# Kernel tuning notes

Hardware: AMD Instinct MI355X
Metric: run time of the kernel (lower is better)

## Reference

```python
import jax, jax.numpy as jnp
import numpy as np

N_NODES = 100_000
N_RAND_EDGES = 3_200_000
IN_FEATS, HIDDEN, N_CLASSES = 256, 32, 40


def setup_inputs() -> dict:
    key = jax.random.key(0)
    kf, ks, kd, kw1, kw2 = jax.random.split(key, 5)
    features = jax.random.normal(kf, (N_NODES, IN_FEATS), dtype=jnp.float32)
    # random edges + explicit self loops (mirrors dgl.add_self_loop)
    src = jnp.concatenate([
        jax.random.randint(ks, (N_RAND_EDGES,), 0, N_NODES, dtype=jnp.int32),
        jnp.arange(N_NODES, dtype=jnp.int32),
    ])
    dst = jnp.concatenate([
        jax.random.randint(kd, (N_RAND_EDGES,), 0, N_NODES, dtype=jnp.int32),
        jnp.arange(N_NODES, dtype=jnp.int32),
    ])
    # Glorot-style init as in DGL GraphConv
    W1 = jax.random.normal(kw1, (IN_FEATS, HIDDEN), dtype=jnp.float32) * (2.0 / (IN_FEATS + HIDDEN)) ** 0.5
    b1 = jnp.zeros((HIDDEN,), dtype=jnp.float32)
    W2 = jax.random.normal(kw2, (HIDDEN, N_CLASSES), dtype=jnp.float32) * (2.0 / (HIDDEN + N_CLASSES)) ** 0.5
    b2 = jnp.zeros((N_CLASSES,), dtype=jnp.float32)
    return {"features": features, "src": src, "dst": dst,
            "W1": W1, "b1": b1, "W2": W2, "b2": b2}


def _graph_conv(x, W, b, src, dst, norm_src, norm_dst):
    """DGL GraphConv, norm='both': D_in^{-1/2} A D_out^{-1/2} X W + b.
    Apply W first (cheaper gather when out_feats small); math-identical."""
    h = (x * norm_src[:, None]) @ W              # [N, out]
    msgs = h[src]                                # gather  [E, out]
    agg = jax.ops.segment_sum(msgs, dst, num_segments=N_NODES)  # scatter-add
    return agg * norm_dst[:, None] + b


def reference(features, src, dst, W1, b1, W2, b2):
    ones = jnp.ones(src.shape[0], dtype=jnp.float32)
    out_deg = jax.ops.segment_sum(ones, src, num_segments=N_NODES)
    in_deg = jax.ops.segment_sum(ones, dst, num_segments=N_NODES)
    norm_src = jax.lax.rsqrt(out_deg)            # self loops guarantee deg >= 1
    norm_dst = jax.lax.rsqrt(in_deg)

    x = _graph_conv(features, W1, b1, src, dst, norm_src, norm_dst)
    x = jax.nn.relu(x)
    # F.dropout(training=self.training) is identity at inference
    x = _graph_conv(x, W2, b2, src, dst, norm_src, norm_dst)
    return jax.nn.log_softmax(x, axis=1)
```

## Files before the change

kernel.cpp:

```cpp
#include <hip/hip_runtime.h>
#include <hip/hip_bf16.h>
#include <math.h>

#define BSHIFT 7
#define NBUCK(N) (((N) + 127) >> 7)
#define TILE 8192
#define CAP 5632
#define CAPS 2040
#define NXCD 8

typedef short bf16x8 __attribute__((ext_vector_type(8)));
typedef float f32x16 __attribute__((ext_vector_type(16)));

__device__ __forceinline__ unsigned short f2bf(float f) {
    unsigned u = __float_as_uint(f);
    u += 0x7fffu + ((u >> 16) & 1u);
    return (unsigned short)(u >> 16);
}
__device__ __forceinline__ unsigned packbf2(float lo, float hi) {
    return (unsigned)f2bf(lo) | ((unsigned)f2bf(hi) << 16);
}
__device__ __forceinline__ float bf_lo(unsigned u) { return __uint_as_float(u << 16); }
__device__ __forceinline__ float bf_hi(unsigned u) { return __uint_as_float(u & 0xffff0000u); }

__device__ __forceinline__ int xcc_id() {
    int x;
    asm volatile("s_getreg_b32 %0, hwreg(HW_REG_XCC_ID)" : "=s"(x));
    return x & (NXCD - 1);
}

__global__ __launch_bounds__(256) void pg_kernel(
    const int* __restrict__ src, const int* __restrict__ dst,
    int* __restrict__ gcurD, int* __restrict__ gcurS,
    int* __restrict__ gbufD, unsigned char* __restrict__ gbufS,
    const float* __restrict__ feat, const float* __restrict__ W1,
    unsigned short* __restrict__ h1, int E, int K, int PB, int N) {
    __shared__ char smem[16896];
    const int t = threadIdx.x;

    if (blockIdx.x < PB) {
        int* cD = (int*)smem;
        int* bD = cD + 800;
        int* cS = bD + 800;
        int* bS = cS + 800;
        const int tile = blockIdx.x * TILE;
        const int vx = xcc_id();
        for (int i = t; i < K; i += 256) { cD[i] = 0; cS[i] = 0; }
        __syncthreads();

        int dv[32];
        #pragma unroll
        for (int i = 0; i < 32; ++i) {
            const int e = tile + i * 256 + t;
            dv[i] = (e < E) ? dst[e] : -1;
            if (dv[i] >= 0) {
                atomicAdd(&cD[dv[i] >> BSHIFT], 1);
                atomicAdd(&cS[src[e] >> BSHIFT], 1);
            }
        }
        __syncthreads();
        for (int i = t; i < K; i += 256) {
            int c = cD[i];
            bD[i] = (c ? atomicAdd(&gcurD[i], c) : 0) + i * CAP;
            cD[i] = 0;
            c = cS[i];
            bS[i] = (c ? atomicAdd(&gcurS[vx * K + i], c) : 0) + (vx * K + i) * CAPS;
            cS[i] = 0;
        }
        __syncthreads();
        #pragma unroll
        for (int i = 0; i < 32; ++i) {
            if (dv[i] >= 0) {
                const int e = tile + i * 256 + t;
                const int sv = src[e];
                const int b1 = dv[i] >> BSHIFT;
                const int p1 = bD[b1] + atomicAdd(&cD[b1], 1);
                gbufD[p1] = ((dv[i] & 127) << 17) | sv;
                const int b2 = sv >> BSHIFT;
                const int p2 = bS[b2] + atomicAdd(&cS[b2], 1);
                gbufS[p2] = (unsigned char)(sv & 127);
            }
        }
    } else {
        short* W1t = (short*)smem;
        for (int i = t; i < 8192; i += 256) {
            const int k = i >> 5, c = i & 31;
            W1t[c * 264 + k] = (short)f2bf(W1[i]);
        }
        __syncthreads();

        const int l  = t & 63;
        const int wv = t >> 6;
        const int base = (blockIdx.x - PB) * 128 + wv * 32;
        const int m  = l & 31;
        const int kh = (l >> 5) << 3;
        int r = base + m;
        if (r >= N) r = N - 1;
        const float* fr = feat + (size_t)r * 256 + kh;
        const short* wr = &W1t[m * 264 + kh];

        f32x16 acc;
        #pragma unroll
        for (int i = 0; i < 16; ++i) acc[i] = 0.f;

        #pragma unroll
        for (int kb = 0; kb < 16; ++kb) {
            const float4 f0 = *(const float4*)(fr + kb * 16);
            const float4 f1 = *(const float4*)(fr + kb * 16 + 4);
            bf16x8 a;
            a[0] = (short)f2bf(f0.x); a[1] = (short)f2bf(f0.y);
            a[2] = (short)f2bf(f0.z); a[3] = (short)f2bf(f0.w);
            a[4] = (short)f2bf(f1.x); a[5] = (short)f2bf(f1.y);
            a[6] = (short)f2bf(f1.z); a[7] = (short)f2bf(f1.w);
            const bf16x8 b = *(const bf16x8*)(wr + kb * 16);
            acc = __builtin_amdgcn_mfma_f32_32x32x16_bf16(a, b, acc, 0, 0, 0);
        }

        const int rbase = base + ((l >> 5) << 2);
        #pragma unroll
        for (int reg = 0; reg < 16; ++reg) {
            const int row = rbase + (reg & 3) + ((reg >> 2) << 3);
            if (row < N)
                h1[(size_t)row * 32 + m] = f2bf(acc[reg]);
        }
    }
}

__global__ __launch_bounds__(256) void fillS_kernel(
    const int* __restrict__ cntS, const unsigned char* __restrict__ gbufS,
    float* __restrict__ nsrc, unsigned* __restrict__ h1, int N, int K) {
    __shared__ int cnt[128];
    __shared__ float sns[128];
    const int t = threadIdx.x;
    const int b = blockIdx.x;
    if (t < 128) cnt[t] = 0;
    __syncthreads();
    for (int x = 0; x < NXCD; ++x) {
        const int seg = x * K + b;
        const int bs = seg * CAPS;
        const int be = bs + min(cntS[seg], CAPS);
        for (int idx = bs + t; idx < be; idx += 256)
            atomicAdd(&cnt[gbufS[idx]], 1);
    }
    __syncthreads();
    if (t < 128) {
        const float v = rsqrtf((float)cnt[t]);
        sns[t] = v;
        const int n = (b << BSHIFT) + t;
        if (n < N) nsrc[n] = v;
    }
    __syncthreads();
    const int node = t >> 1;
    const int n = (b << BSHIFT) + node;
    if (n < N) {
        const float ns = sns[node];
        unsigned* row = h1 + (size_t)n * 16 + (t & 1) * 8;
        uint4 q0 = *(uint4*)row;
        uint4 q1 = *(uint4*)(row + 4);
        q0.x = packbf2(bf_lo(q0.x) * ns, bf_hi(q0.x) * ns);
        q0.y = packbf2(bf_lo(q0.y) * ns, bf_hi(q0.y) * ns);
        q0.z = packbf2(bf_lo(q0.z) * ns, bf_hi(q0.z) * ns);
        q0.w = packbf2(bf_lo(q0.w) * ns, bf_hi(q0.w) * ns);
        q1.x = packbf2(bf_lo(q1.x) * ns, bf_hi(q1.x) * ns);
        q1.y = packbf2(bf_lo(q1.y) * ns, bf_hi(q1.y) * ns);
        q1.z = packbf2(bf_lo(q1.z) * ns, bf_hi(q1.z) * ns);
        q1.w = packbf2(bf_lo(q1.w) * ns, bf_hi(q1.w) * ns);
        *(uint4*)row = q0;
        *(uint4*)(row + 4) = q1;
    }
}

__global__ __launch_bounds__(512) void fda1_kernel(
    const int* __restrict__ cntD, int* __restrict__ gbufD,
    const unsigned* __restrict__ h1, const float* __restrict__ nsrc,
    const float* __restrict__ b1, int* __restrict__ rowstart,
    int* __restrict__ indeg, float* __restrict__ ndst,
    unsigned* __restrict__ x1s, int N, int K) {
    __shared__ int lraw[CAP];
    __shared__ int lcsr[CAP];
    __shared__ int cnt[512], sc[512], cur[512];
    __shared__ float sb1[32];
    const int t = threadIdx.x;
    const int b = blockIdx.x;
    if (t < 512) cnt[t] = 0;
    if (t < 32) sb1[t] = b1[t];
    __syncthreads();

    const int bs = b * CAP;
    const int total = min(cntD[b], CAP);
    for (int i = t; i < total; i += 512) {
        const int v = gbufD[bs + i];
        lraw[i] = v;
        const int key = ((v >> 17) << 2) | ((v & 131071) >> 15);
        atomicAdd(&cnt[key], 1);
    }
    __syncthreads();
    sc[t] = cnt[t];
    __syncthreads();
    for (int off = 1; off < 512; off <<= 1) {
        int x = (t >= off) ? sc[t - off] : 0;
        __syncthreads();
        sc[t] += x;
        __syncthreads();
    }
    cur[t] = sc[t] - cnt[t];
    if (t < 128) {
        const int rsl = sc[4 * t] - cnt[4 * t];
        const int deg = sc[4 * t + 3] - rsl;
        const int n = (b << BSHIFT) + t;
        if (n < N) {
            rowstart[n] = bs + rsl;
            indeg[n] = deg;
            ndst[n] = rsqrtf((float)max(deg, 1));
        }
    }
    __syncthreads();
    for (int i = t; i < total; i += 512) {
        const int v = lraw[i];
        const int key = ((v >> 17) << 2) | ((v & 131071) >> 15);
        const int pos = atomicAdd(&cur[key], 1);
        lcsr[pos] = v & 131071;
    }
    __syncthreads();
    for (int i = t; i < total; i += 512) gbufD[bs + i] = lcsr[i];

    const int c  = t & 3;
    const int eg = (t >> 2) & 1;
    const uint4* H = (const uint4*)h1;
    for (int half = 0; half < 2; ++half) {
        const int node = (t >> 3) + half * 64;
        const int n = (b << BSHIFT) + node;
        if (n >= N) continue;
        const int rs = sc[4 * node] - cnt[4 * node];
        const int re = sc[4 * node + 3];
        const int deg = re - rs;
        const int n8 = deg >> 3;
        float a0=0.f,a1=0.f,a2=0.f,a3=0.f,a4=0.f,a5=0.f,a6=0.f,a7=0.f;
        float d0=0.f,d1=0.f,d2=0.f,d3=0.f,d4=0.f,d5=0.f,d6=0.f,d7=0.f;
        for (int i = 0; i < n8; ++i) {
            const int k0 = rs + i * 8 + eg * 4;
            const int s0 = lcsr[k0],     s1 = lcsr[k0 + 1];
            const int s2 = lcsr[k0 + 2], s3 = lcsr[k0 + 3];
            const uint4 q0 = H[(size_t)s0 * 4 + c];
            const uint4 q1 = H[(size_t)s1 * 4 + c];
            const uint4 q2 = H[(size_t)s2 * 4 + c];
            const uint4 q3 = H[(size_t)s3 * 4 + c];
            a0 += bf_lo(q0.x); a1 += bf_hi(q0.x);
            a2 += bf_lo(q0.y); a3 += bf_hi(q0.y);
            a4 += bf_lo(q0.z); a5 += bf_hi(q0.z);
            a6 += bf_lo(q0.w); a7 += bf_hi(q0.w);
            d0 += bf_lo(q1.x); d1 += bf_hi(q1.x);
            d2 += bf_lo(q1.y); d3 += bf_hi(q1.y);
            d4 += bf_lo(q1.z); d5 += bf_hi(q1.z);
            d6 += bf_lo(q1.w); d7 += bf_hi(q1.w);
            a0 += bf_lo(q2.x); a1 += bf_hi(q2.x);
            a2 += bf_lo(q2.y); a3 += bf_hi(q2.y);
            a4 += bf_lo(q2.z); a5 += bf_hi(q2.z);
            a6 += bf_lo(q2.w); a7 += bf_hi(q2.w);
            d0 += bf_lo(q3.x); d1 += bf_hi(q3.x);
            d2 += bf_lo(q3.y); d3 += bf_hi(q3.y);
            d4 += bf_lo(q3.z); d5 += bf_hi(q3.z);
            d6 += bf_lo(q3.w); d7 += bf_hi(q3.w);
        }
        for (int k = rs + n8 * 8 + eg; k < re; k += 2) {
            const int s0 = lcsr[k];
            const uint4 q0 = H[(size_t)s0 * 4 + c];
            a0 += bf_lo(q0.x); a1 += bf_hi(q0.x);
            a2 += bf_lo(q0.y); a3 += bf_hi(q0.y);
            a4 += bf_lo(q0.z); a5 += bf_hi(q0.z);
            a6 += bf_lo(q0.w); a7 += bf_hi(q0.w);
        }
        a0 += d0; a1 += d1; a2 += d2; a3 += d3;
        a4 += d4; a5 += d5; a6 += d6; a7 += d7;
        a0 += __shfl_xor(a0, 4, 64); a1 += __shfl_xor(a1, 4, 64);
        a2 += __shfl_xor(a2, 4, 64); a3 += __shfl_xor(a3, 4, 64);
        a4 += __shfl_xor(a4, 4, 64); a5 += __shfl_xor(a5, 4, 64);
        a6 += __shfl_xor(a6, 4, 64); a7 += __shfl_xor(a7, 4, 64);
        if (eg == 0) {
            const float nd = rsqrtf((float)max(deg, 1));
            const float ns = nsrc[n];
            const float* bb = sb1 + c * 8;
            float x0 = fmaxf(a0 * nd + bb[0], 0.f) * ns;
            float x1 = fmaxf(a1 * nd + bb[1], 0.f) * ns;
            float x2 = fmaxf(a2 * nd + bb[2], 0.f) * ns;
            float x3 = fmaxf(a3 * nd + bb[3], 0.f) * ns;
            float x4 = fmaxf(a4 * nd + bb[4], 0.f) * ns;
            float x5 = fmaxf(a5 * nd + bb[5], 0.f) * ns;
            float x6 = fmaxf(a6 * nd + bb[6], 0.f) * ns;
            float x7 = fmaxf(a7 * nd + bb[7], 0.f) * ns;
            uint4 o;
            o.x = packbf2(x0, x1); o.y = packbf2(x2, x3);
            o.z = packbf2(x4, x5); o.w = packbf2(x6, x7);
            ((uint4*)x1s)[(size_t)n * 4 + c] = o;
        }
    }
}

__global__ __launch_bounds__(256) void agg2f_kernel(
    const int* __restrict__ csr_src, const int* __restrict__ rowstart,
    const int* __restrict__ indeg, const unsigned* __restrict__ x1s,
    const float* __restrict__ ndst, const float* __restrict__ W2,
    const float* __restrict__ b2, float* __restrict__ out, int N) {
    __shared__ float sW2[32 * 40];
    __shared__ float sb2[40];
    const int t = threadIdx.x;
    for (int i = t; i < 1280; i += 256) sW2[i] = W2[i];
    if (t < 40) sb2[t] = b2[t];
    __syncthreads();
    const int n = blockIdx.x * 32 + (t >> 3);
    if (n >= N) return;
    const int c  = t & 3;
    const int eg = (t >> 2) & 1;
    const int rs = rowstart[n];
    const int deg = indeg[n];
    const int re = rs + deg;
    const int n8 = deg >> 3;
    float a0=0.f,a1=0.f,a2=0.f,a3=0.f,a4=0.f,a5=0.f,a6=0.f,a7=0.f;
    float d0=0.f,d1=0.f,d2=0.f,d3=0.f,d4=0.f,d5=0.f,d6=0.f,d7=0.f;
    const uint4* H = (const uint4*)x1s;
    for (int i = 0; i < n8; ++i) {
        const int k0 = rs + i * 8 + eg * 4;
        const int s0 = csr_src[k0],     s1 = csr_src[k0 + 1];
        const int s2 = csr_src[k0 + 2], s3 = csr_src[k0 + 3];
        const uint4 q0 = H[(size_t)s0 * 4 + c];
        const uint4 q1 = H[(size_t)s1 * 4 + c];
        const uint4 q2 = H[(size_t)s2 * 4 + c];
        const uint4 q3 = H[(size_t)s3 * 4 + c];
        a0 += bf_lo(q0.x); a1 += bf_hi(q0.x);
        a2 += bf_lo(q0.y); a3 += bf_hi(q0.y);
        a4 += bf_lo(q0.z); a5 += bf_hi(q0.z);
        a6 += bf_lo(q0.w); a7 += bf_hi(q0.w);
        d0 += bf_lo(q1.x); d1 += bf_hi(q1.x);
        d2 += bf_lo(q1.y); d3 += bf_hi(q1.y);
        d4 += bf_lo(q1.z); d5 += bf_hi(q1.z);
        d6 += bf_lo(q1.w); d7 += bf_hi(q1.w);
        a0 += bf_lo(q2.x); a1 += bf_hi(q2.x);
        a2 += bf_lo(q2.y); a3 += bf_hi(q2.y);
        a4 += bf_lo(q2.z); a5 += bf_hi(q2.z);
        a6 += bf_lo(q2.w); a7 += bf_hi(q2.w);
        d0 += bf_lo(q3.x); d1 += bf_hi(q3.x);
        d2 += bf_lo(q3.y); d3 += bf_hi(q3.y);
        d4 += bf_lo(q3.z); d5 += bf_hi(q3.z);
        d6 += bf_lo(q3.w); d7 += bf_hi(q3.w);
    }
    for (int k = rs + n8 * 8 + eg; k < re; k += 2) {
        const int s0 = csr_src[k];
        const uint4 q0 = H[(size_t)s0 * 4 + c];
        a0 += bf_lo(q0.x); a1 += bf_hi(q0.x);
        a2 += bf_lo(q0.y); a3 += bf_hi(q0.y);
        a4 += bf_lo(q0.z); a5 += bf_hi(q0.z);
        a6 += bf_lo(q0.w); a7 += bf_hi(q0.w);
    }
    a0 += d0; a1 += d1; a2 += d2; a3 += d3;
    a4 += d4; a5 += d5; a6 += d6; a7 += d7;
    a0 += __shfl_xor(a0, 4, 64); a1 += __shfl_xor(a1, 4, 64);
    a2 += __shfl_xor(a2, 4, 64); a3 += __shfl_xor(a3, 4, 64);
    a4 += __shfl_xor(a4, 4, 64); a5 += __shfl_xor(a5, 4, 64);
    a6 += __shfl_xor(a6, 4, 64); a7 += __shfl_xor(a7, 4, 64);
    const float nd = ndst[n];
    const float v0 = a0 * nd, v1 = a1 * nd, v2 = a2 * nd, v3 = a3 * nd;
    const float v4 = a4 * nd, v5 = a5 * nd, v6 = a6 * nd, v7 = a7 * nd;

    const int j = t & 7;
    float z[5];
    #pragma unroll
    for (int u = 0; u < 5; ++u) z[u] = sb2[j * 5 + u];
    const int gbase = (t & 63) & ~7;
    #pragma unroll
    for (int cc = 0; cc < 4; ++cc) {
        const int sl = gbase + cc;
        const float w0 = __shfl(v0, sl, 64);
        const float w1 = __shfl(v1, sl, 64);
        const float w2 = __shfl(v2, sl, 64);
        const float w3 = __shfl(v3, sl, 64);
        const float w4 = __shfl(v4, sl, 64);
        const float w5 = __shfl(v5, sl, 64);
        const float w6 = __shfl(v6, sl, 64);
        const float w7 = __shfl(v7, sl, 64);
        const float* Wr = &sW2[(cc * 8) * 40 + j * 5];
        #pragma unroll
        for (int u = 0; u < 5; ++u) {
            z[u] += w0 * Wr[u]       + w1 * Wr[40 + u]  + w2 * Wr[80 + u]  + w3 * Wr[120 + u]
                  + w4 * Wr[160 + u] + w5 * Wr[200 + u] + w6 * Wr[240 + u] + w7 * Wr[280 + u];
        }
    }
    float m = z[0];
    #pragma unroll
    for (int u = 1; u < 5; ++u) m = fmaxf(m, z[u]);
    m = fmaxf(m, __shfl_xor(m, 1, 64));
    m = fmaxf(m, __shfl_xor(m, 2, 64));
    m = fmaxf(m, __shfl_xor(m, 4, 64));
    float s = 0.f;
    #pragma unroll
    for (int u = 0; u < 5; ++u) s += __expf(z[u] - m);
    s += __shfl_xor(s, 1, 64);
    s += __shfl_xor(s, 2, 64);
    s += __shfl_xor(s, 4, 64);
    const float ls = __logf(s);
    float* op = out + (size_t)n * 40 + j * 5;
    #pragma unroll
    for (int u = 0; u < 5; ++u) op[u] = z[u] - m - ls;
}

extern "C" void kernel_launch(void* const* d_in, const int* in_sizes, int n_in,
                              void* d_out, int out_size, void* d_ws, size_t ws_size,
                              hipStream_t stream) {
    const float* feat = (const float*)d_in[0];
    const int*   src  = (const int*)d_in[1];
    const int*   dst  = (const int*)d_in[2];
    const float* W1   = (const float*)d_in[3];
    const float* b1   = (const float*)d_in[4];
    const float* W2   = (const float*)d_in[5];
    const float* b2   = (const float*)d_in[6];
    float* out = (float*)d_out;

    const int N = in_sizes[0] / 256;
    const int E = in_sizes[1];
    const int K = NBUCK(N);

    char* p = (char*)d_ws;
    float* nsrc = (float*)p;                 p += (size_t)N * 4;
    float* ndst = (float*)p;                 p += (size_t)N * 4;
    unsigned* h1  = (unsigned*)p;            p += (size_t)N * 64;
    unsigned* x1s = (unsigned*)p;            p += (size_t)N * 64;
    char* a2dead = (char*)p;                 p += (size_t)N * 128;
    int* rowstart = (int*)p;                 p += (size_t)N * 4;
    int* indeg_i  = (int*)p;                 p += (size_t)N * 4;
    int* gcurD    = (int*)p;                 p += 800 * 4;
    int* gcurS    = (int*)p;                 p += (size_t)NXCD * 800 * 4;
    int* gbufD    = (int*)p;                 p += (size_t)K * CAP * 4;
    unsigned char* gbufS = (unsigned char*)a2dead;

    hipMemsetAsync(gcurD, 0, sizeof(int) * (800 + NXCD * 800), stream);

    const int PB = (E + TILE - 1) / TILE;
    const int GB = (N + 127) / 128;

    pg_kernel<<<PB + GB, 256, 0, stream>>>(src, dst, gcurD, gcurS, gbufD, gbufS,
                                           feat, W1, (unsigned short*)h1, E, K, PB, N);
    fillS_kernel<<<K, 256, 0, stream>>>(gcurS, gbufS, nsrc, h1, N, K);
    fda1_kernel<<<K, 512, 0, stream>>>(gcurD, gbufD, h1, nsrc, b1,
                                       rowstart, indeg_i, ndst, x1s, N, K);
    agg2f_kernel<<<(N + 31) / 32, 256, 0, stream>>>(gbufD, rowstart, indeg_i, x1s, ndst, W2, b2, out, N);
}
```

Baseline: 338.6 us.

## Stage bucketed edge scatter in LDS before coalesced global copy

The partition blocks now do a local prefix scan over bucket counts and place each tile's edges in bucket order in LDS, then copy each bucket's run to the global buffers with wave-wide contiguous writes. Before, each edge was written straight to a scattered global position. The aim is to turn random global stores into coalesced ones. The cost is a much larger shared allocation (about 62KB), which lowers occupancy for both the partition and the GEMM branches, plus extra scan barriers.

Result: slower. 379.9 us (+12.2%).

```diff
diff --git a/kernel.cpp b/kernel.cpp
--- a/kernel.cpp
+++ b/kernel.cpp
@@ -35,17 +35,23 @@
     int* __restrict__ gbufD, unsigned char* __restrict__ gbufS,
     const float* __restrict__ feat, const float* __restrict__ W1,
     unsigned short* __restrict__ h1, int E, int K, int PB, int N) {
-    __shared__ char smem[16896];
+    __shared__ char smem[62208];
     const int t = threadIdx.x;
 
     if (blockIdx.x < PB) {
-        int* cD = (int*)smem;
-        int* bD = cD + 800;
-        int* cS = bD + 800;
-        int* bS = cS + 800;
+        int* ldsD  = (int*)smem;
+        unsigned char* ldsS = (unsigned char*)(smem + 32768);
+        int* cntD  = (int*)(smem + 40960);
+        int* scanD = (int*)(smem + 44160);
+        int* shfD  = (int*)(smem + 47360);
+        int* cntS  = (int*)(smem + 50560);
+        int* scanS = (int*)(smem + 53760);
+        int* shfS  = (int*)(smem + 56960);
+        int* tsD   = (int*)(smem + 60160);
+        int* tsS   = (int*)(smem + 61184);
         const int tile = blockIdx.x * TILE;
         const int vx = xcc_id();
-        for (int i = t; i < K; i += 256) { cD[i] = 0; cS[i] = 0; }
+        for (int i = t; i < 800; i += 256) { cntD[i] = 0; cntS[i] = 0; }
         __syncthreads();
 
         int dv[32];
@@ -54,18 +60,47 @@
             const int e = tile + i * 256 + t;
             dv[i] = (e < E) ? dst[e] : -1;
             if (dv[i] >= 0) {
-                atomicAdd(&cD[dv[i] >> BSHIFT], 1);
-                atomicAdd(&cS[src[e] >> BSHIFT], 1);
+                atomicAdd(&cntD[dv[i] >> BSHIFT], 1);
+                atomicAdd(&cntS[src[e] >> BSHIFT], 1);
             }
         }
         __syncthreads();
+
+        int l0 = 0, l1 = 0, l2 = 0, l3 = 0, m0 = 0, m1 = 0, m2 = 0, m3 = 0;
+        if (t < 200) {
+            const int b4 = t * 4;
+            l0 = cntD[b4]; l1 = cntD[b4 + 1]; l2 = cntD[b4 + 2]; l3 = cntD[b4 + 3];
+            m0 = cntS[b4]; m1 = cntS[b4 + 1]; m2 = cntS[b4 + 2]; m3 = cntS[b4 + 3];
+        }
+        tsD[t] = l0 + l1 + l2 + l3;
+        tsS[t] = m0 + m1 + m2 + m3;
+        __syncthreads();
+        for (int off = 1; off < 256; off <<= 1) {
+            const int a = (t >= off) ? tsD[t - off] : 0;
+            const int b = (t >= off) ? tsS[t - off] : 0;
+            __syncthreads();
+            tsD[t] += a; tsS[t] += b;
+            __syncthreads();
+        }
+        if (t < 200) {
+            const int b4 = t * 4;
+            const int baseD = (t > 0) ? tsD[t - 1] : 0;
+            const int baseS = (t > 0) ? tsS[t - 1] : 0;
+            scanD[b4] = baseD;               scanD[b4 + 1] = baseD + l0;
+            scanD[b4 + 2] = baseD + l0 + l1; scanD[b4 + 3] = baseD + l0 + l1 + l2;
+            scanS[b4] = baseS;               scanS[b4 + 1] = baseS + m0;
+            scanS[b4 + 2] = baseS + m0 + m1; scanS[b4 + 3] = baseS + m0 + m1 + m2;
+        }
+        __syncthreads();
         for (int i = t; i < K; i += 256) {
-            int c = cD[i];
-            bD[i] = (c ? atomicAdd(&gcurD[i], c) : 0) + i * CAP;
-            cD[i] = 0;
-            c = cS[i];
-            bS[i] = (c ? atomicAdd(&gcurS[vx * K + i], c) : 0) + (vx * K + i) * CAPS;
-            cS[i] = 0;
+            int c = cntD[i];
+            int gb = (c ? atomicAdd(&gcurD[i], c) : 0) + i * CAP;
+            shfD[i] = gb - scanD[i];
+            cntD[i] = 0;
+            c = cntS[i];
+            gb = (c ? atomicAdd(&gcurS[vx * K + i], c) : 0) + (vx * K + i) * CAPS;
+            shfS[i] = gb - scanS[i];
+            cntS[i] = 0;
         }
         __syncthreads();
         #pragma unroll
@@ -74,12 +109,24 @@
                 const int e = tile + i * 256 + t;
                 const int sv = src[e];
                 const int b1 = dv[i] >> BSHIFT;
-                const int p1 = bD[b1] + atomicAdd(&cD[b1], 1);
-                gbufD[p1] = ((dv[i] & 127) << 17) | sv;
+                const int p1 = scanD[b1] + atomicAdd(&cntD[b1], 1);
+                ldsD[p1] = ((dv[i] & 127) << 17) | sv;
                 const int b2 = sv >> BSHIFT;
-                const int p2 = bS[b2] + atomicAdd(&cS[b2], 1);
-                gbufS[p2] = (unsigned char)(sv & 127);
+                const int p2 = scanS[b2] + atomicAdd(&cntS[b2], 1);
+                ldsS[p2] = (unsigned char)(sv & 127);
             }
+        }
+        __syncthreads();
+        const int wid = t >> 6, lane = t & 63;
+        for (int b = wid; b < K; b += 4) {
+            const int len = cntD[b], st = scanD[b], gb = shfD[b] + st;
+            for (int off = lane; off < len; off += 64)
+                gbufD[gb + off] = ldsD[st + off];
+        }
+        for (int b = wid; b < K; b += 4) {
+            const int len = cntS[b], st = scanS[b], gb = shfS[b] + st;
+            for (int off = lane; off < len; off += 64)
+                gbufS[gb + off] = ldsS[st + off];
         }
     } else {
         short* W1t = (short*)smem;
```
